# Kernel tuning notes

Measured on AMD Instinct MI355X. Metric: run time of the kernel, lower is better.

Reference implementation:

```python
import jax, jax.numpy as jnp
import numpy as np

HEADS = 16

def setup_inputs() -> dict:
    key = jax.random.key(0)
    ks = jax.random.split(key, 7)
    B, S, E = 2, 2048, 1024
    return {
        "query": jax.random.normal(ks[0], (B, S, E), dtype=jnp.float32),
        "key": jax.random.normal(ks[1], (B, S, E), dtype=jnp.float32),
        "value": jax.random.normal(ks[2], (B, S, E), dtype=jnp.float32),
        "Wqkv": jax.random.normal(ks[3], (E, 3 * E), dtype=jnp.float32) * (E ** -0.5),
        "bqkv": jax.random.normal(ks[4], (3 * E,), dtype=jnp.float32) * 0.02,
        "Wproj": jax.random.normal(ks[5], (E, E), dtype=jnp.float32) * (E ** -0.5),
        "bproj": jax.random.normal(ks[6], (E,), dtype=jnp.float32) * 0.02,
    }

def reference(query, key, value, Wqkv, bqkv, Wproj, bproj):
    # key/value args are unused in the original forward (overwritten by QKV split)
    B, S, E = query.shape
    H = HEADS
    hd = E // H
    qkv = query @ Wqkv + bqkv                     # [B, S, 3E]
    qkv = qkv.reshape(B, S, H, 3 * hd).transpose(0, 2, 1, 3)  # [B, H, S, 3hd]
    q = qkv[..., :hd]
    k = qkv[..., hd:2 * hd]
    v = qkv[..., 2 * hd:]
    qk = jnp.einsum("bhqd,bhkd->bhqk", q, k)
    # faithful quirk: original divides by head_dim**-0.5, i.e. multiplies by sqrt(hd)
    scaled = qk / (hd ** -0.5)
    attn = jax.nn.softmax(scaled, axis=-1)        # dropout p=0 -> identity
    out = jnp.einsum("bhqk,bhkd->bhqd", attn, v)  # [B, H, S, hd]
    out = out.transpose(0, 2, 1, 3).reshape(B, S, E)
    return out @ Wproj + bproj
```

## Files before the change

### kernel.cpp

```cpp
#include <hip/hip_runtime.h>
#include <hip/hip_bf16.h>
#include <stdint.h>

typedef __attribute__((ext_vector_type(8))) _Float16 f16x8;
typedef __attribute__((ext_vector_type(4))) _Float16 f16x4;
typedef __attribute__((ext_vector_type(4))) float f32x4;

static constexpr int BATCH = 2;
static constexpr int SEQ = 2048;
static constexpr int EMB = 1024;
static constexpr int NH = 16;
static constexpr int HD_ = 64;

#define AS1 __attribute__((address_space(1)))
#define AS3 __attribute__((address_space(3)))

__device__ __forceinline__ void gload_lds16(const void* g, void* l) {
  __builtin_amdgcn_global_load_lds((const AS1 uint32_t*)g, (AS3 uint32_t*)l, 16, 0, 0);
}

__device__ __forceinline__ f32x4 mfma16(f16x8 a, f16x8 b, f32x4 c) {
  return __builtin_amdgcn_mfma_f32_16x16x32_f16(a, b, c, 0, 0, 0);
}

__device__ __forceinline__ f16x8 swzread(const _Float16* base, int row, int blk) {
  return *(const f16x8*)((const char*)base + row * 128 +
                         ((blk * 16) ^ ((row & 7) << 4)));
}

__global__ __launch_bounds__(256) void k_prep(const float* __restrict__ q,
                                              _Float16* __restrict__ qo,
                                              const float* __restrict__ wqkv,
                                              _Float16* __restrict__ wqkvo,
                                              const float* __restrict__ wproj,
                                              _Float16* __restrict__ wprojo) {
  __shared__ float tile[32][33];
  const int blk = blockIdx.x;
  const int t = threadIdx.x;
  if (blk < 4096) {
    const int idx = blk * 256 + t;
    float4 v = reinterpret_cast<const float4*>(q)[idx];
    const float* f = reinterpret_cast<const float*>(&v);
    _Float16 h[4];
#pragma unroll
    for (int i = 0; i < 4; ++i) h[i] = (_Float16)f[i];
    reinterpret_cast<uint2*>(qo)[idx] = *reinterpret_cast<uint2*>(h);
    return;
  }
  const float* in;
  _Float16* out;
  int R, C, bx, by;
  bool perm;
  if (blk < 4096 + 3072) {
    const int lo = blk - 4096;
    bx = lo % 96;
    by = lo / 96;
    in = wqkv; out = wqkvo; R = 1024; C = 3072; perm = true;
  } else {
    const int lo = blk - 7168;
    bx = lo & 31;
    by = lo >> 5;
    in = wproj; out = wprojo; R = 1024; C = 1024; perm = false;
  }
  const int tr = t >> 5, tc = t & 31;
  const int r0 = by * 32, c0 = bx * 32;
#pragma unroll
  for (int rr = 0; rr < 32; rr += 8)
    tile[tr + rr][tc] = in[(size_t)(r0 + tr + rr) * C + c0 + tc];
  __syncthreads();
#pragma unroll
  for (int rr = 0; rr < 32; rr += 8) {
    const int c = c0 + tr + rr;
    int d = c;
    if (perm) {
      const int h = c / 192, r = c - h * 192;
      d = (r < 64) ? h * 64 + r
                   : (r < 128 ? 1024 + h * 64 + (r - 64) : 2048 + h * 64 + (r - 128));
    }
    out[(size_t)d * R + r0 + tc] = (_Float16)tile[tc][tr + rr];
  }
}

__global__ __launch_bounds__(256) void k_gemm_qkv(const _Float16* __restrict__ A,
                                                  const _Float16* __restrict__ Bt,
                                                  const float* __restrict__ bias,
                                                  _Float16* __restrict__ oq,
                                                  _Float16* __restrict__ ok,
                                                  _Float16* __restrict__ ov) {
  constexpr int K = EMB;
  __shared__ _Float16 As[2][128 * 32];
  __shared__ _Float16 Bs[2][128 * 32];
  const int t = threadIdx.x;
  const int l = t & 63, w = t >> 6;
  const int lr = l & 15, lg = l >> 4;
  const int wr = w >> 1, wc = w & 1;
  const int id = blockIdx.x;
  const int xcd = id & 7, wg = id >> 3;
  const int mq = xcd & 3, ng = xcd >> 2;
  const int mi = wg / 12, ni = wg % 12;
  const int m0 = (mq * 8 + mi) * 128;
  const int n0 = (ng * 12 + ni) * 128;

  auto stage = [&](int buf, int k0) {
#pragma unroll
    for (int j = 0; j < 2; ++j) {
      const int c = t + 256 * j;
      const int row = c >> 2, cb = c & 3;
      gload_lds16(A + (size_t)(m0 + row) * K + k0 + cb * 8, &As[buf][c * 8]);
      gload_lds16(Bt + (size_t)(n0 + row) * K + k0 + cb * 8, &Bs[buf][c * 8]);
    }
  };

  f32x4 acc[4][4];
#pragma unroll
  for (int m = 0; m < 4; ++m)
#pragma unroll
    for (int n = 0; n < 4; ++n) acc[m][n] = f32x4{0.f, 0.f, 0.f, 0.f};

  stage(0, 0);
  const int NT = K / 32;
  int cur = 0;
  for (int kt = 0; kt < NT; ++kt) {
    __syncthreads();
    if (kt + 1 < NT) stage(cur ^ 1, (kt + 1) * 32);
    f16x8 af[4], bf[4];
#pragma unroll
    for (int m = 0; m < 4; ++m)
      af[m] = *(const f16x8*)&As[cur][(wr * 64 + m * 16 + lr) * 32 + lg * 8];
#pragma unroll
    for (int n = 0; n < 4; ++n)
      bf[n] = *(const f16x8*)&Bs[cur][(wc * 64 + n * 16 + lr) * 32 + lg * 8];
#pragma unroll
    for (int m = 0; m < 4; ++m)
#pragma unroll
      for (int n = 0; n < 4; ++n) acc[m][n] = mfma16(af[m], bf[n], acc[m][n]);
    cur ^= 1;
  }

  const int sec = n0 >> 10;
#pragma unroll
  for (int m = 0; m < 4; ++m) {
#pragma unroll
    for (int n = 0; n < 4; ++n) {
      const int col = n0 + wc * 64 + n * 16 + lr;
      const int cc = col & 1023;
      const int h = cc >> 6, r = cc & 63;
      const float bv = bias[h * 192 + sec * 64 + r];
      const int row0 = m0 + wr * 64 + m * 16 + lg * 4;
      const int b = row0 >> 11, s0 = row0 & (SEQ - 1);
      if (sec == 2) {
        f16x4 vv;
#pragma unroll
        for (int i = 0; i < 4; ++i) vv[i] = (_Float16)(acc[m][n][i] + bv);
        *(f16x4*)&ov[(((size_t)b * NH + h) * HD_ + r) * SEQ + s0] = vv;
      } else {
#pragma unroll
        for (int i = 0; i < 4; ++i) {
          const float v = acc[m][n][i] + bv;
          const size_t dst = (((size_t)b * NH + h) * SEQ + s0 + i) * HD_ + r;
          if (sec == 0)
            oq[dst] = (_Float16)(v * 11.5415603f);
          else
            ok[dst] = (_Float16)v;
        }
      }
    }
  }
}

__global__ __launch_bounds__(256) void k_gemm_proj(const _Float16* __restrict__ A,
                                                   const _Float16* __restrict__ Bt,
                                                   const float* __restrict__ bias,
                                                   float* __restrict__ of) {
  constexpr int K = EMB, N = EMB;
  __shared__ _Float16 As[2][128 * 32];
  __shared__ _Float16 Bs[2][128 * 32];
  const int t = threadIdx.x;
  const int l = t & 63, w = t >> 6;
  const int lr = l & 15, lg = l >> 4;
  const int wr = w >> 1, wc = w & 1;
  const int id = blockIdx.x;
  const int xcd = id & 7, wg = id >> 3;
  const int m0 = (xcd * 4 + wg / 8) * 128;
  const int n0 = (wg & 7) * 128;

  auto stage = [&](int buf, int k0) {
#pragma unroll
    for (int j = 0; j < 2; ++j) {
      const int c = t + 256 * j;
      const int row = c >> 2, cb = c & 3;
      gload_lds16(A + (size_t)(m0 + row) * K + k0 + cb * 8, &As[buf][c * 8]);
      gload_lds16(Bt + (size_t)(n0 + row) * K + k0 + cb * 8, &Bs[buf][c * 8]);
    }
  };

  f32x4 acc[4][4];
#pragma unroll
  for (int m = 0; m < 4; ++m)
#pragma unroll
    for (int n = 0; n < 4; ++n) acc[m][n] = f32x4{0.f, 0.f, 0.f, 0.f};

  stage(0, 0);
  const int NT = K / 32;
  int cur = 0;
  for (int kt = 0; kt < NT; ++kt) {
    __syncthreads();
    if (kt + 1 < NT) stage(cur ^ 1, (kt + 1) * 32);
    f16x8 af[4], bf[4];
#pragma unroll
    for (int m = 0; m < 4; ++m)
      af[m] = *(const f16x8*)&As[cur][(wr * 64 + m * 16 + lr) * 32 + lg * 8];
#pragma unroll
    for (int n = 0; n < 4; ++n)
      bf[n] = *(const f16x8*)&Bs[cur][(wc * 64 + n * 16 + lr) * 32 + lg * 8];
#pragma unroll
    for (int m = 0; m < 4; ++m)
#pragma unroll
      for (int n = 0; n < 4; ++n) acc[m][n] = mfma16(af[m], bf[n], acc[m][n]);
    cur ^= 1;
  }

#pragma unroll
  for (int m = 0; m < 4; ++m)
#pragma unroll
    for (int n = 0; n < 4; ++n)
#pragma unroll
      for (int i = 0; i < 4; ++i) {
        const int row = m0 + wr * 64 + m * 16 + lg * 4 + i;
        const int col = n0 + wc * 64 + n * 16 + lr;
        of[(size_t)row * N + col] = acc[m][n][i] + bias[col];
      }
}

__global__ __launch_bounds__(512) void k_attn(const _Float16* __restrict__ qs,
                                              const _Float16* __restrict__ ks,
                                              const _Float16* __restrict__ vt,
                                              _Float16* __restrict__ ao) {
  __shared__ _Float16 Kt[3][64][64];
  __shared__ _Float16 Vt[3][64][64];
  __shared__ _Float16 Pl[8][16][64];
  const int t = threadIdx.x;
  const int l = t & 63, w = t >> 6;
  const int lr = l & 15, lg = l >> 4;
  const int id = blockIdx.x;
  const int xc = id & 7, m_ = id >> 3;
  const int bh = xc + 8 * (m_ >> 4);
  const int qb = (m_ & 15) * 128 + w * 16;

  const size_t qoff = ((size_t)bh * SEQ + qb + lr) * HD_;
  const f16x8 qf0 = *(const f16x8*)(qs + qoff + lg * 8);
  const f16x8 qf1 = *(const f16x8*)(qs + qoff + 32 + lg * 8);

  const _Float16* kbase = ks + (size_t)bh * SEQ * HD_;
  const _Float16* vbase = vt + (size_t)bh * HD_ * SEQ;

  const int srow = t >> 3, scb = t & 7;
  auto stage = [&](const int buf, const int kv0) {
    gload_lds16(kbase + (size_t)(kv0 + srow) * HD_ + (scb ^ (srow & 7)) * 8,
                &Kt[buf][srow][scb * 8]);
    gload_lds16(vbase + (size_t)srow * SEQ + kv0 + (scb ^ (srow & 7)) * 8,
                &Vt[buf][srow][scb * 8]);
  };

  stage(0, 0);
  stage(1, 64);

  float mr = -1e30f, lsum = 0.f;
  f32x4 oacc[4];
#pragma unroll
  for (int n = 0; n < 4; ++n) oacc[n] = f32x4{0.f, 0.f, 0.f, 0.f};

  const int NT = SEQ / 64;
  int cur = 0;
  for (int it = 0; it < NT; ++it) {
    if (it == NT - 1)
      asm volatile("s_waitcnt vmcnt(0)" ::: "memory");
    else
      asm volatile("s_waitcnt vmcnt(2)" ::: "memory");
    __builtin_amdgcn_s_barrier();
    if (it + 2 < NT) {
      int nb = cur + 2;
      if (nb >= 3) nb -= 3;
      stage(nb, (it + 2) * 64);
    }

    f32x4 sa[4];
    __builtin_amdgcn_s_setprio(1);
#pragma unroll
    for (int t4 = 0; t4 < 4; ++t4) {
      const int r = t4 * 16 + lr;
      const f16x8 kf0 = swzread(&Kt[cur][0][0], r, lg);
      const f16x8 kf1 = swzread(&Kt[cur][0][0], r, lg + 4);
      f32x4 s = mfma16(kf0, qf0, f32x4{0.f, 0.f, 0.f, 0.f});
      sa[t4] = mfma16(kf1, qf1, s);
    }
    __builtin_amdgcn_s_setprio(0);

    float t01 = fmaxf(fmaxf(sa[0][0], sa[0][1]), fmaxf(sa[0][2], sa[0][3]));
    float t23 = fmaxf(fmaxf(sa[1][0], sa[1][1]), fmaxf(sa[1][2], sa[1][3]));
    float t45 = fmaxf(fmaxf(sa[2][0], sa[2][1]), fmaxf(sa[2][2], sa[2][3]));
    float t67 = fmaxf(fmaxf(sa[3][0], sa[3][1]), fmaxf(sa[3][2], sa[3][3]));
    float tm = fmaxf(fmaxf(t01, t23), fmaxf(t45, t67));
    tm = fmaxf(tm, __shfl_xor(tm, 16));
    tm = fmaxf(tm, __shfl_xor(tm, 32));

    if (__all(tm < mr - 24.0f)) {
      cur = (cur + 1 == 3) ? 0 : cur + 1;
      continue;
    }

    if (__any(tm > mr + 8.0f)) {
      const float nm = fmaxf(mr, tm);
      const float corr = exp2f(mr - nm);
      mr = nm;
      lsum *= corr;
      float cb4[4];
#pragma unroll
      for (int i = 0; i < 4; ++i)
        cb4[i] = __shfl(corr, (l & 48) + ((l >> 4) << 2) + i);
#pragma unroll
      for (int n = 0; n < 4; ++n)
#pragma unroll
        for (int i = 0; i < 4; ++i) oacc[n][i] *= cb4[i];
    }

    float ts = 0.f;
    char* plbase = (char*)&Pl[w][0][0];
#pragma unroll
    for (int t4 = 0; t4 < 4; ++t4) {
      f16x4 pp;
#pragma unroll
      for (int i = 0; i < 4; ++i) {
        const float p = exp2f(sa[t4][i] - mr);
        ts += p;
        pp[i] = (_Float16)p;
      }
      *(f16x4*)(plbase + lr * 128 + ((t4 * 32 + lg * 8) ^ ((lr & 7) << 4))) = pp;
    }
    ts += __shfl_xor(ts, 16);
    ts += __shfl_xor(ts, 32);
    lsum += ts;

    const f16x8 aP0 = swzread(&Pl[w][0][0], lr, lg);
    const f16x8 aP1 = swzread(&Pl[w][0][0], lr, lg + 4);
    __builtin_amdgcn_s_setprio(1);
#pragma unroll
    for (int n = 0; n < 4; ++n) {
      const int d = n * 16 + lr;
      const f16x8 bv0 = swzread(&Vt[cur][0][0], d, lg);
      const f16x8 bv1 = swzread(&Vt[cur][0][0], d, lg + 4);
      oacc[n] = mfma16(aP0, bv0, oacc[n]);
      oacc[n] = mfma16(aP1, bv1, oacc[n]);
    }
    __builtin_amdgcn_s_setprio(0);

    cur = (cur + 1 == 3) ? 0 : cur + 1;
  }

  float ls4[4];
#pragma unroll
  for (int i = 0; i < 4; ++i)
    ls4[i] = __shfl(lsum, (l & 48) + ((l >> 4) << 2) + i);
  const int b = bh >> 4, h = bh & 15;
#pragma unroll
  for (int n = 0; n < 4; ++n)
#pragma unroll
    for (int i = 0; i < 4; ++i) {
      const int row = qb + ((l >> 4) << 2) + i;
      ao[((size_t)b * SEQ + row) * EMB + h * HD_ + n * 16 + lr] =
          (_Float16)(oacc[n][i] / ls4[i]);
    }
}

extern "C" void kernel_launch(void* const* d_in, const int* in_sizes, int n_in,
                              void* d_out, int out_size, void* d_ws, size_t ws_size,
                              hipStream_t stream) {
  const float* query = (const float*)d_in[0];
  const float* Wqkv = (const float*)d_in[3];
  const float* bqkv = (const float*)d_in[4];
  const float* Wproj = (const float*)d_in[5];
  const float* bproj = (const float*)d_in[6];
  float* out = (float*)d_out;

  char* ws = (char*)d_ws;
  const size_t MB = 1024 * 1024;
  _Float16* q_f16   = (_Float16*)(ws + 0);
  _Float16* Wqkv_t  = (_Float16*)(ws + 16 * MB);
  _Float16* q_s     = (_Float16*)(ws + 24 * MB);
  _Float16* k_s     = (_Float16*)(ws + 32 * MB);
  _Float16* v_t     = (_Float16*)(ws + 40 * MB);
  _Float16* Wproj_t = (_Float16*)(ws + 48 * MB);
  _Float16* a_o     = (_Float16*)(ws + 51 * MB);

  const int M = BATCH * SEQ;
  k_prep<<<dim3(8192), 256, 0, stream>>>(query, q_f16, Wqkv, Wqkv_t, Wproj, Wproj_t);
  k_gemm_qkv<<<dim3(768), 256, 0, stream>>>(q_f16, Wqkv_t, bqkv, q_s, k_s, v_t);
  k_attn<<<dim3(512), 512, 0, stream>>>(q_s, k_s, v_t, a_o);
  k_gemm_proj<<<dim3(256), 256, 0, stream>>>(a_o, Wproj_t, bproj, out);
}
```

Baseline: 145.4 us.

## Restructure QKV GEMM into 256x256 tiles with swizzled LDS and phased pipelining

The QKV projection GEMM now uses 256x256 output tiles per 512-thread block (8 waves) with K-step 64, so each block covers four times the previous tile area. LDS tiles are XOR-swizzled to avoid bank conflicts, and loads for the next K-tile are issued in four phases interleaved with MFMA work, using explicit vmcnt waits, barriers and setprio. This is meant to raise arithmetic intensity and hide global-load latency. The trade-off is only 192 blocks for the 256 CUs and higher register and LDS pressure.

```diff
diff --git a/kernel.cpp b/kernel.cpp
--- a/kernel.cpp
+++ b/kernel.cpp
@@ -81,82 +81,126 @@
   }
 }
 
-__global__ __launch_bounds__(256) void k_gemm_qkv(const _Float16* __restrict__ A,
-                                                  const _Float16* __restrict__ Bt,
-                                                  const float* __restrict__ bias,
-                                                  _Float16* __restrict__ oq,
-                                                  _Float16* __restrict__ ok,
-                                                  _Float16* __restrict__ ov) {
+__global__ __launch_bounds__(512, 1) void k_gemm_qkv(const _Float16* __restrict__ A,
+                                                     const _Float16* __restrict__ Bt,
+                                                     const float* __restrict__ bias,
+                                                     _Float16* __restrict__ oq,
+                                                     _Float16* __restrict__ ok,
+                                                     _Float16* __restrict__ ov) {
   constexpr int K = EMB;
-  __shared__ _Float16 As[2][128 * 32];
-  __shared__ _Float16 Bs[2][128 * 32];
+  __shared__ _Float16 As[2][2][128 * 64];
+  __shared__ _Float16 Bs[2][2][128 * 64];
   const int t = threadIdx.x;
   const int l = t & 63, w = t >> 6;
   const int lr = l & 15, lg = l >> 4;
-  const int wr = w >> 1, wc = w & 1;
+  const int wm = w >> 2, wn = w & 3;
   const int id = blockIdx.x;
   const int xcd = id & 7, wg = id >> 3;
-  const int mq = xcd & 3, ng = xcd >> 2;
-  const int mi = wg / 12, ni = wg % 12;
-  const int m0 = (mq * 8 + mi) * 128;
-  const int n0 = (ng * 12 + ni) * 128;
-
-  auto stage = [&](int buf, int k0) {
-#pragma unroll
-    for (int j = 0; j < 2; ++j) {
-      const int c = t + 256 * j;
-      const int row = c >> 2, cb = c & 3;
-      gload_lds16(A + (size_t)(m0 + row) * K + k0 + cb * 8, &As[buf][c * 8]);
-      gload_lds16(Bt + (size_t)(n0 + row) * K + k0 + cb * 8, &Bs[buf][c * 8]);
-    }
+  const int m0 = (xcd * 2 + wg / 12) * 256;
+  const int n0 = (wg % 12) * 256;
+
+  const int sr0 = t >> 3, scb = t & 7;
+  auto stageA = [&](int buf, int half, int kt) {
+    const _Float16* g = A + (size_t)(m0 + half * 128) * K + kt * 64;
+    _Float16* d = &As[buf][half][0];
+    gload_lds16(g + (size_t)sr0 * K + (scb ^ (sr0 & 7)) * 8, d + sr0 * 64 + scb * 8);
+    const int r1 = sr0 + 64;
+    gload_lds16(g + (size_t)r1 * K + (scb ^ (r1 & 7)) * 8, d + r1 * 64 + scb * 8);
   };
-
-  f32x4 acc[4][4];
-#pragma unroll
-  for (int m = 0; m < 4; ++m)
+  auto stageB = [&](int buf, int half, int kt) {
+    const _Float16* g = Bt + (size_t)(n0 + half * 128) * K + kt * 64;
+    _Float16* d = &Bs[buf][half][0];
+    gload_lds16(g + (size_t)sr0 * K + (scb ^ (sr0 & 7)) * 8, d + sr0 * 64 + scb * 8);
+    const int r1 = sr0 + 64;
+    gload_lds16(g + (size_t)r1 * K + (scb ^ (r1 & 7)) * 8, d + r1 * 64 + scb * 8);
+  };
+
+  f32x4 acc[8][4];
+#pragma unroll
+  for (int m = 0; m < 8; ++m)
 #pragma unroll
     for (int n = 0; n < 4; ++n) acc[m][n] = f32x4{0.f, 0.f, 0.f, 0.f};
 
-  stage(0, 0);
-  const int NT = K / 32;
-  int cur = 0;
-  for (int kt = 0; kt < NT; ++kt) {
-    __syncthreads();
-    if (kt + 1 < NT) stage(cur ^ 1, (kt + 1) * 32);
-    f16x8 af[4], bf[4];
-#pragma unroll
-    for (int m = 0; m < 4; ++m)
-      af[m] = *(const f16x8*)&As[cur][(wr * 64 + m * 16 + lr) * 32 + lg * 8];
-#pragma unroll
-    for (int n = 0; n < 4; ++n)
-      bf[n] = *(const f16x8*)&Bs[cur][(wc * 64 + n * 16 + lr) * 32 + lg * 8];
-#pragma unroll
-    for (int m = 0; m < 4; ++m)
-#pragma unroll
-      for (int n = 0; n < 4; ++n) acc[m][n] = mfma16(af[m], bf[n], acc[m][n]);
-    cur ^= 1;
+  stageA(0, 0, 0);
+  stageA(0, 1, 0);
+  stageB(0, 0, 0);
+  stageB(0, 1, 0);
+
+  const int bhh = wn >> 1, brow0 = (wn & 1) * 64;
+  f16x8 bf[4][2];
+
+  for (int pair = 0; pair < 8; ++pair) {
+#pragma unroll
+    for (int ph = 0; ph < 8; ++ph) {
+      const int buf = ph >> 2, q = ph & 3;
+      bool issued = true;
+      if (ph < 4) {
+        const int kt = 2 * pair + 1;
+        if (q == 0) stageA(1, 0, kt);
+        else if (q == 1) stageA(1, 1, kt);
+        else if (q == 2) stageB(1, 0, kt);
+        else stageB(1, 1, kt);
+      } else if (pair + 1 < 8) {
+        const int kt = 2 * pair + 2;
+        if (q == 0) stageA(0, 0, kt);
+        else if (q == 1) stageA(0, 1, kt);
+        else if (q == 2) stageB(0, 0, kt);
+        else stageB(0, 1, kt);
+      } else {
+        issued = false;
+      }
+      if (q == 0) {
+        if (issued)
+          asm volatile("s_waitcnt vmcnt(2)" ::: "memory");
+        else
+          asm volatile("s_waitcnt vmcnt(0)" ::: "memory");
+        __builtin_amdgcn_s_barrier();
+#pragma unroll
+        for (int nf = 0; nf < 4; ++nf)
+#pragma unroll
+          for (int ks = 0; ks < 2; ++ks)
+            bf[nf][ks] = swzread(&Bs[buf][bhh][0], brow0 + nf * 16 + lr, ks * 4 + lg);
+      }
+      f16x8 af[2][2];
+#pragma unroll
+      for (int dm = 0; dm < 2; ++dm)
+#pragma unroll
+        for (int ks = 0; ks < 2; ++ks)
+          af[dm][ks] = swzread(&As[buf][wm][0], (q * 2 + dm) * 16 + lr, ks * 4 + lg);
+      __builtin_amdgcn_s_setprio(1);
+#pragma unroll
+      for (int dm = 0; dm < 2; ++dm)
+#pragma unroll
+        for (int nf = 0; nf < 4; ++nf)
+#pragma unroll
+          for (int ks = 0; ks < 2; ++ks)
+            acc[q * 2 + dm][nf] =
+                mfma16(af[dm][ks], bf[nf][ks], acc[q * 2 + dm][nf]);
+      __builtin_amdgcn_s_setprio(0);
+      __builtin_amdgcn_s_barrier();
+    }
   }
 
   const int sec = n0 >> 10;
 #pragma unroll
-  for (int m = 0; m < 4; ++m) {
-#pragma unroll
-    for (int n = 0; n < 4; ++n) {
-      const int col = n0 + wc * 64 + n * 16 + lr;
+  for (int mf = 0; mf < 8; ++mf) {
+#pragma unroll
+    for (int nf = 0; nf < 4; ++nf) {
+      const int col = n0 + wn * 64 + nf * 16 + lr;
       const int cc = col & 1023;
       const int h = cc >> 6, r = cc & 63;
       const float bv = bias[h * 192 + sec * 64 + r];
-      const int row0 = m0 + wr * 64 + m * 16 + lg * 4;
+      const int row0 = m0 + wm * 128 + mf * 16 + lg * 4;
       const int b = row0 >> 11, s0 = row0 & (SEQ - 1);
       if (sec == 2) {
         f16x4 vv;
 #pragma unroll
-        for (int i = 0; i < 4; ++i) vv[i] = (_Float16)(acc[m][n][i] + bv);
+        for (int i = 0; i < 4; ++i) vv[i] = (_Float16)(acc[mf][nf][i] + bv);
         *(f16x4*)&ov[(((size_t)b * NH + h) * HD_ + r) * SEQ + s0] = vv;
       } else {
 #pragma unroll
         for (int i = 0; i < 4; ++i) {
-          const float v = acc[m][n][i] + bv;
+          const float v = acc[mf][nf][i] + bv;
           const size_t dst = (((size_t)b * NH + h) * SEQ + s0 + i) * HD_ + r;
           if (sec == 0)
             oq[dst] = (_Float16)(v * 11.5415603f);
@@ -394,7 +438,7 @@
 
   const int M = BATCH * SEQ;
   k_prep<<<dim3(8192), 256, 0, stream>>>(query, q_f16, Wqkv, Wqkv_t, Wproj, Wproj_t);
-  k_gemm_qkv<<<dim3(768), 256, 0, stream>>>(q_f16, Wqkv_t, bqkv, q_s, k_s, v_t);
+  k_gemm_qkv<<<dim3(192), 512, 0, stream>>>(q_f16, Wqkv_t, bqkv, q_s, k_s, v_t);
   k_attn<<<dim3(512), 512, 0, stream>>>(q_s, k_s, v_t, a_o);
   k_gemm_proj<<<dim3(256), 256, 0, stream>>>(a_o, Wproj_t, bproj, out);
 }
```

After: 145.1 us. No clear change (-0.2%).
